# Performance work log

Measured on AMD Instinct MI355X. Metric: run time of the kernel, lower is better.

## Reference

```python
import jax, jax.numpy as jnp
import numpy as np

N_NODES = 50000
N_EDGES = 800000
D_IN = 64
D_HID = 64
N_LAYERS = 3
BN_EPS = 1e-5


def setup_inputs() -> dict:
    key = jax.random.key(0)
    ks = jax.random.split(key, 10)
    x = jax.random.normal(ks[0], (N_NODES, D_IN), dtype=jnp.float32)
    edge_index = jax.random.randint(ks[1], (2, N_EDGES), 0, N_NODES, dtype=jnp.int32)
    # Per-layer GCN weights (in==hid==64 so we can stack) and BatchNorm params.
    Ws = jax.random.normal(ks[2], (N_LAYERS, D_HID, D_HID), dtype=jnp.float32) / np.sqrt(D_HID)
    bs = jnp.zeros((N_LAYERS, D_HID), dtype=jnp.float32)
    gammas = jnp.ones((N_LAYERS, D_HID), dtype=jnp.float32)
    betas = jnp.zeros((N_LAYERS, D_HID), dtype=jnp.float32)
    means = jax.random.normal(ks[3], (N_LAYERS, D_HID), dtype=jnp.float32) * 0.1
    variances = jax.random.uniform(ks[4], (N_LAYERS, D_HID), dtype=jnp.float32, minval=0.5, maxval=1.5)
    lin_w = jax.random.normal(ks[5], (D_HID, 1), dtype=jnp.float32) / np.sqrt(D_HID)
    lin_b = jnp.zeros((1,), dtype=jnp.float32)
    return {"x": x, "edge_index": edge_index, "Ws": Ws, "bs": bs,
            "gammas": gammas, "betas": betas, "means": means,
            "variances": variances, "lin_w": lin_w, "lin_b": lin_b}


def _gnn_forward(x, edge_index, Ws, bs, gammas, betas, means, variances, lin_w, lin_b):
    n = x.shape[0]
    # GCNConv: add self loops, symmetric D^{-1/2}(A+I)D^{-1/2} normalization.
    loop = jnp.arange(n, dtype=edge_index.dtype)
    row = jnp.concatenate([edge_index[0], loop])  # source nodes
    col = jnp.concatenate([edge_index[1], loop])  # target nodes
    deg = jax.ops.segment_sum(jnp.ones(row.shape[0], x.dtype), col, num_segments=n)
    dinv = jax.lax.rsqrt(jnp.maximum(deg, 1.0))  # deg >= 1 from self loops
    norm = (dinv[row] * dinv[col])[:, None]  # [E+N, 1]

    h = x
    for i in range(N_LAYERS):
        h = h @ Ws[i]  # transform first (PyG GCNConv order)
        h = jax.ops.segment_sum(h[row] * norm, col, num_segments=n) + bs[i]
        # BatchNorm1d (eval mode: running stats) + ReLU; dropout is identity in eval.
        h = (h - means[i]) * jax.lax.rsqrt(variances[i] + BN_EPS) * gammas[i] + betas[i]
        h = jax.nn.relu(h)
    out = h @ lin_w + lin_b  # [N, 1]
    return out[:, 0]


def reference(x, edge_index, Ws, bs, gammas, betas, means, variances, lin_w, lin_b):
    return _gnn_forward(x, edge_index, Ws, bs, gammas, betas, means, variances, lin_w, lin_b)
```

## Files before the change

kernel.cpp:

```cpp
#include <hip/hip_runtime.h>
#include <hip/hip_bf16.h>
#include <hip/hip_fp16.h>


#define BN_EPS 1e-5f
#define CAP 64
#define CHUNK 4096
#define SEGCAP 5120
#define NBINS_MAX 256

__global__ __launch_bounds__(256) void k_bin_pairs(const int* __restrict__ row,
                                                   const int* __restrict__ col,
                                                   int* __restrict__ gfill,
                                                   unsigned int* __restrict__ gpairs,
                                                   int e, int nbins) {
    __shared__ unsigned int pl[CHUNK];
    __shared__ int bcnt[NBINS_MAX];
    __shared__ int bbase[NBINS_MAX];
    int tid = threadIdx.x;
    int base = blockIdx.x * CHUNK;
    for (int b = tid; b < nbins; b += 256) bcnt[b] = 0;
    __syncthreads();
    int nloc = e - base; if (nloc > CHUNK) nloc = CHUNK;
    #pragma unroll
    for (int it = 0; it < CHUNK / 1024; ++it) {
        int le = (it * 256 + tid) * 4;
        if (le + 3 < nloc) {
            int i4 = (base >> 2) + it * 256 + tid;
            int4 r = ((const int4*)row)[i4];
            int4 c = ((const int4*)col)[i4];
            atomicAdd(&bcnt[c.x >> 8], 1); pl[le + 0] = (unsigned)r.x | ((unsigned)c.x << 16);
            atomicAdd(&bcnt[c.y >> 8], 1); pl[le + 1] = (unsigned)r.y | ((unsigned)c.y << 16);
            atomicAdd(&bcnt[c.z >> 8], 1); pl[le + 2] = (unsigned)r.z | ((unsigned)c.z << 16);
            atomicAdd(&bcnt[c.w >> 8], 1); pl[le + 3] = (unsigned)r.w | ((unsigned)c.w << 16);
        } else {
            for (int j = 0; j < 4; ++j) {
                if (le + j < nloc) {
                    int rr = row[base + le + j];
                    int cc = col[base + le + j];
                    atomicAdd(&bcnt[cc >> 8], 1);
                    pl[le + j] = (unsigned)rr | ((unsigned)cc << 16);
                }
            }
        }
    }
    __syncthreads();
    for (int b = tid; b < nbins; b += 256) {
        bbase[b] = atomicAdd(&gfill[b], bcnt[b]);
        bcnt[b] = 0;
    }
    __syncthreads();
    for (int i = tid; i < nloc; i += 256) {
        unsigned int p = pl[i];
        int bin = p >> 24;
        int off = atomicAdd(&bcnt[bin], 1);
        int pos = bbase[bin] + off;
        if (pos < SEGCAP) gpairs[(size_t)bin * SEGCAP + pos] = p;
    }
}

__global__ __launch_bounds__(256) void k_bucket_build(const unsigned int* __restrict__ gpairs,
                                                      const int* __restrict__ gfill,
                                                      int* __restrict__ cnt,
                                                      unsigned short* __restrict__ bucket,
                                                      int n) {
    __shared__ unsigned short lb[256 * CAP];
    __shared__ int lc[256];
    int tid = threadIdx.x;
    int bin = blockIdx.x;
    lc[tid] = 0;
    __syncthreads();
    int m = gfill[bin]; if (m > SEGCAP) m = SEGCAP;
    const unsigned int* seg = gpairs + (size_t)bin * SEGCAP;
    for (int i = tid; i < m; i += 256) {
        unsigned int p = seg[i];
        int src = p & 0xffff;
        int dl = (p >> 16) & 255;
        int pos = atomicAdd(&lc[dl], 1);
        if (pos < CAP) lb[dl * CAP + pos] = (unsigned short)src;
    }
    __syncthreads();
    int nodebase = bin << 8;
    const int4* lb4 = (const int4*)lb;
    int4* gb4 = (int4*)bucket;
    for (int i = tid; i < 256 * 8; i += 256) {
        int rrow = i >> 3;
        int gnode = nodebase + rrow;
        if (gnode < n) gb4[(size_t)gnode * 8 + (i & 7)] = lb4[i];
    }
    int gnode = nodebase + tid;
    if (gnode < n) cnt[gnode] = lc[tid];
}

__device__ __forceinline__ void mm_core(const float* at, const float* wsh,
                                        __half* out, int rbase, int n, int tid) {
    int r = tid >> 2;
    int cg = tid & 3;
    float4 a0 = {0, 0, 0, 0}, a1 = a0, a2 = a0, a3 = a0;
    const float4* W4 = (const float4*)wsh;
    #pragma unroll 8
    for (int k = 0; k < 64; ++k) {
        float hv = at[k * 65 + r];
        float4 w0 = W4[k * 16 + cg * 4 + 0];
        float4 w1 = W4[k * 16 + cg * 4 + 1];
        float4 w2 = W4[k * 16 + cg * 4 + 2];
        float4 w3 = W4[k * 16 + cg * 4 + 3];
        a0.x = fmaf(hv, w0.x, a0.x); a0.y = fmaf(hv, w0.y, a0.y);
        a0.z = fmaf(hv, w0.z, a0.z); a0.w = fmaf(hv, w0.w, a0.w);
        a1.x = fmaf(hv, w1.x, a1.x); a1.y = fmaf(hv, w1.y, a1.y);
        a1.z = fmaf(hv, w1.z, a1.z); a1.w = fmaf(hv, w1.w, a1.w);
        a2.x = fmaf(hv, w2.x, a2.x); a2.y = fmaf(hv, w2.y, a2.y);
        a2.z = fmaf(hv, w2.z, a2.z); a2.w = fmaf(hv, w2.w, a2.w);
        a3.x = fmaf(hv, w3.x, a3.x); a3.y = fmaf(hv, w3.y, a3.y);
        a3.z = fmaf(hv, w3.z, a3.z); a3.w = fmaf(hv, w3.w, a3.w);
    }
    int gr = rbase + r;
    if (gr < n) {
        union { __half2 h2[4]; uint4 u; } o1, o2;
        o1.h2[0] = __floats2half2_rn(a0.x, a0.y);
        o1.h2[1] = __floats2half2_rn(a0.z, a0.w);
        o1.h2[2] = __floats2half2_rn(a1.x, a1.y);
        o1.h2[3] = __floats2half2_rn(a1.z, a1.w);
        o2.h2[0] = __floats2half2_rn(a2.x, a2.y);
        o2.h2[1] = __floats2half2_rn(a2.z, a2.w);
        o2.h2[2] = __floats2half2_rn(a3.x, a3.y);
        o2.h2[3] = __floats2half2_rn(a3.z, a3.w);
        uint4* op = (uint4*)(out + (size_t)gr * 64 + cg * 16);
        op[0] = o1.u; op[1] = o2.u;
    }
}

template<int LAYER>
__global__ __launch_bounds__(256) void k_mm(const __half* __restrict__ A,
                                            const float* __restrict__ W,
                                            __half* __restrict__ out, int n) {
    __shared__ float at[64 * 65];
    __shared__ float wsh[64 * 64];
    int tid = threadIdx.x;
    int rbase = blockIdx.x * 64;
    for (int i = tid; i < 4096; i += 256) wsh[i] = W[i];
    for (int i = tid; i < 2048; i += 256) {
        int r = i >> 5;
        int c2 = (i & 31) * 2;
        int gr = rbase + r;
        float2 v = {0.f, 0.f};
        if (gr < n) v = __half22float2(*(const __half2*)(A + (size_t)gr * 64 + c2));
        at[c2 * 65 + r] = v.x;
        at[(c2 + 1) * 65 + r] = v.y;
    }
    __syncthreads();
    mm_core(at, wsh, out, rbase, n, tid);
}

__global__ __launch_bounds__(256) void k_mm0(const float* __restrict__ A,
                                             const float* __restrict__ W,
                                             const int* __restrict__ cnt,
                                             __half* __restrict__ out, int n) {
    __shared__ float at[64 * 65];
    __shared__ float wsh[64 * 64];
    __shared__ float dl[64];
    int tid = threadIdx.x;
    int rbase = blockIdx.x * 64;
    if (tid < 64) {
        int gr = rbase + tid;
        dl[tid] = (gr < n) ? rsqrtf((float)(cnt[gr] + 1)) : 0.f;
    }
    for (int i = tid; i < 4096; i += 256) wsh[i] = W[i];
    __syncthreads();
    for (int i = tid; i < 1024; i += 256) {
        int r = i >> 4;
        int c4 = (i & 15) * 4;
        int gr = rbase + r;
        float4 v = {0.f, 0.f, 0.f, 0.f};
        if (gr < n) v = *(const float4*)(A + (size_t)gr * 64 + c4);
        float d = dl[r];
        at[(c4 + 0) * 65 + r] = v.x * d;
        at[(c4 + 1) * 65 + r] = v.y * d;
        at[(c4 + 2) * 65 + r] = v.z * d;
        at[(c4 + 3) * 65 + r] = v.w * d;
    }
    __syncthreads();
    mm_core(at, wsh, out, rbase, n, tid);
}

template<int LAYER, bool FINAL>
__global__ __launch_bounds__(256, 6) void k_agg(const __half* __restrict__ t,
                                                const int* __restrict__ cnt,
                                                const unsigned short* __restrict__ bucket,
                                                const float* __restrict__ bias,
                                                const float* __restrict__ gamma,
                                                const float* __restrict__ beta,
                                                const float* __restrict__ mean,
                                                const float* __restrict__ var,
                                                __half* __restrict__ hout,
                                                const float* __restrict__ lw,
                                                const float* __restrict__ lb,
                                                float* __restrict__ outp, int n) {
    int lane = threadIdx.x & 63;
    int g = lane >> 3;
    int q = lane & 7;
    int qo = q << 3;
    float S[8], O[8], LW[8];
    #pragma unroll
    for (int i = 0; i < 8; ++i) {
        int f = qo + i;
        float s = gamma[f] * rsqrtf(var[f] + BN_EPS);
        S[i] = s;
        O[i] = fmaf(bias[f] - mean[f], s, beta[f]);
        if (FINAL) LW[i] = lw[f];
    }
    int wave = (blockIdx.x * blockDim.x + threadIdx.x) >> 6;
    int nwaves = (gridDim.x * blockDim.x) >> 6;
    union HV { float4 f4; __half2 h2[4]; };
    for (int node = wave; node < n; node += nwaves) {
        int c = cnt[node];
        int myidx = (int)bucket[node * CAP + lane];
        HV vself;
        vself.f4 = *(const float4*)(t + ((size_t)node << 6) + qo);
        float acc[8] = {0.f, 0.f, 0.f, 0.f, 0.f, 0.f, 0.f, 0.f};
        int cm1 = c - 1;
        for (int sub = 0; sub < c; sub += 16) {
            int j1 = sub + g;
            int j2 = sub + 8 + g;
            int i1 = __shfl(myidx, (j1 < cm1 ? j1 : cm1), 64);
            int i2 = __shfl(myidx, (j2 < cm1 ? j2 : cm1), 64);
            float m1 = (j1 < c) ? 1.f : 0.f;
            float m2 = (j2 < c) ? 1.f : 0.f;
            HV v1, v2;
            v1.f4 = *(const float4*)(t + ((size_t)i1 << 6) + qo);
            v2.f4 = *(const float4*)(t + ((size_t)i2 << 6) + qo);
            #pragma unroll
            for (int p = 0; p < 4; ++p) {
                float2 a = __half22float2(v1.h2[p]);
                float2 b = __half22float2(v2.h2[p]);
                acc[2 * p]     = fmaf(m1, a.x, acc[2 * p]);
                acc[2 * p + 1] = fmaf(m1, a.y, acc[2 * p + 1]);
                acc[2 * p]     = fmaf(m2, b.x, acc[2 * p]);
                acc[2 * p + 1] = fmaf(m2, b.y, acc[2 * p + 1]);
            }
        }
        {
            float ms = (g == 0) ? 1.f : 0.f;
            #pragma unroll
            for (int p = 0; p < 4; ++p) {
                float2 a = __half22float2(vself.h2[p]);
                acc[2 * p]     = fmaf(ms, a.x, acc[2 * p]);
                acc[2 * p + 1] = fmaf(ms, a.y, acc[2 * p + 1]);
            }
        }
        #pragma unroll
        for (int i = 0; i < 8; ++i) {
            acc[i] += __shfl_down(acc[i], 32, 64);
            acc[i] += __shfl_down(acc[i], 16, 64);
            acc[i] += __shfl_down(acc[i], 8, 64);
        }
        float di = rsqrtf((float)(c + 1));
        if (FINAL) {
            float p = 0.f;
            #pragma unroll
            for (int i = 0; i < 8; ++i) {
                float h = fmaxf(fmaf(acc[i] * di, S[i], O[i]), 0.f);
                p = fmaf(h, LW[i], p);
            }
            p += __shfl_down(p, 4, 64);
            p += __shfl_down(p, 2, 64);
            p += __shfl_down(p, 1, 64);
            if (lane == 0) outp[node] = p + lb[0];
        } else if (g == 0) {
            union { __half2 h2[4]; uint4 u; } o;
            #pragma unroll
            for (int i = 0; i < 4; ++i) {
                float h0 = fmaxf(fmaf(acc[2 * i] * di, S[2 * i], O[2 * i]), 0.f);
                float h1 = fmaxf(fmaf(acc[2 * i + 1] * di, S[2 * i + 1], O[2 * i + 1]), 0.f);
                o.h2[i] = __floats2half2_rn(h0 * di, h1 * di);
            }
            *(uint4*)(hout + ((size_t)node << 6) + qo) = o.u;
        }
    }
}

extern "C" void kernel_launch(void* const* d_in, const int* in_sizes, int n_in,
                              void* d_out, int out_size, void* d_ws, size_t ws_size,
                              hipStream_t stream) {
    const float* x    = (const float*)d_in[0];
    const int*   ei   = (const int*)d_in[1];
    const float* Ws   = (const float*)d_in[2];
    const float* bs   = (const float*)d_in[3];
    const float* gam  = (const float*)d_in[4];
    const float* bet  = (const float*)d_in[5];
    const float* mean = (const float*)d_in[6];
    const float* var  = (const float*)d_in[7];
    const float* lw   = (const float*)d_in[8];
    const float* lb   = (const float*)d_in[9];
    float* out = (float*)d_out;

    const int n = in_sizes[0] / 64;
    const int e = in_sizes[1] / 2;
    const int* row = ei;
    const int* col = ei + e;
    const int nbins = (n + 255) >> 8;

    int* ws_i = (int*)d_ws;
    int* cnt = ws_i;
    int* gfill = ws_i + n;
    unsigned short* bucket = (unsigned short*)(ws_i + n + 256);
    __half* t16 = (__half*)(ws_i + n + 256 + 32 * (size_t)n);
    __half* h16 = t16 + 64 * (size_t)n;
    unsigned int* gpairs = (unsigned int*)t16;

    int nb_p1 = (e + CHUNK - 1) / CHUNK;
    int nb_mm = (n + 63) / 64;
    int nb_ag = 2048;

    hipMemsetAsync(gfill, 0, 256 * sizeof(int), stream);
    k_bin_pairs<<<nb_p1, 256, 0, stream>>>(row, col, gfill, gpairs, e, nbins);
    k_bucket_build<<<nbins, 256, 0, stream>>>(gpairs, gfill, cnt, bucket, n);

    k_mm0<<<nb_mm, 256, 0, stream>>>(x, Ws, cnt, t16, n);
    k_agg<0, false><<<nb_ag, 256, 0, stream>>>(t16, cnt, bucket,
                                               bs, gam, bet, mean, var,
                                               h16, nullptr, nullptr, nullptr, n);
    k_mm<1><<<nb_mm, 256, 0, stream>>>(h16, Ws + 4096, t16, n);
    k_agg<1, false><<<nb_ag, 256, 0, stream>>>(t16, cnt, bucket,
                                               bs + 64, gam + 64, bet + 64, mean + 64, var + 64,
                                               h16, nullptr, nullptr, nullptr, n);
    k_mm<2><<<nb_mm, 256, 0, stream>>>(h16, Ws + 8192, t16, n);
    k_agg<2, true><<<nb_ag, 256, 0, stream>>>(t16, cnt, bucket,
                                              bs + 128, gam + 128, bet + 128, mean + 128, var + 128,
                                              nullptr, lw, lb, out, n);
}
```

Before: 230.3 us.

## Replace scalar FMA node-transform GEMMs with split-fp16 MFMA kernels

Replaces the shared-memory scalar-FMA 64x64 transform kernels with a matrix-core kernel using 16x16x32 fp16 MFMA instructions. A small prep kernel converts each layer's weights to transposed hi/lo fp16 pairs, and the first layer also splits the fp32 input into hi/lo to keep near-fp32 accuracy. This removes the LDS staging and transpose and cuts the per-row FMA work. The cost is extra MFMAs for the split precision, scalar fp16 output stores, and per-lane weight fragments read from global memory.

```diff
diff --git a/kernel.cpp b/kernel.cpp
--- a/kernel.cpp
+++ b/kernel.cpp
@@ -8,6 +8,9 @@
 #define CHUNK 4096
 #define SEGCAP 5120
 #define NBINS_MAX 256
+
+typedef _Float16 f16x8 __attribute__((ext_vector_type(8)));
+typedef float f32x4 __attribute__((ext_vector_type(4)));
 
 __global__ __launch_bounds__(256) void k_bin_pairs(const int* __restrict__ row,
                                                    const int* __restrict__ col,
@@ -92,95 +95,97 @@
     if (gnode < n) cnt[gnode] = lc[tid];
 }
 
-__device__ __forceinline__ void mm_core(const float* at, const float* wsh,
-                                        __half* out, int rbase, int n, int tid) {
-    int r = tid >> 2;
-    int cg = tid & 3;
-    float4 a0 = {0, 0, 0, 0}, a1 = a0, a2 = a0, a3 = a0;
-    const float4* W4 = (const float4*)wsh;
-    #pragma unroll 8
-    for (int k = 0; k < 64; ++k) {
-        float hv = at[k * 65 + r];
-        float4 w0 = W4[k * 16 + cg * 4 + 0];
-        float4 w1 = W4[k * 16 + cg * 4 + 1];
-        float4 w2 = W4[k * 16 + cg * 4 + 2];
-        float4 w3 = W4[k * 16 + cg * 4 + 3];
-        a0.x = fmaf(hv, w0.x, a0.x); a0.y = fmaf(hv, w0.y, a0.y);
-        a0.z = fmaf(hv, w0.z, a0.z); a0.w = fmaf(hv, w0.w, a0.w);
-        a1.x = fmaf(hv, w1.x, a1.x); a1.y = fmaf(hv, w1.y, a1.y);
-        a1.z = fmaf(hv, w1.z, a1.z); a1.w = fmaf(hv, w1.w, a1.w);
-        a2.x = fmaf(hv, w2.x, a2.x); a2.y = fmaf(hv, w2.y, a2.y);
-        a2.z = fmaf(hv, w2.z, a2.z); a2.w = fmaf(hv, w2.w, a2.w);
-        a3.x = fmaf(hv, w3.x, a3.x); a3.y = fmaf(hv, w3.y, a3.y);
-        a3.z = fmaf(hv, w3.z, a3.z); a3.w = fmaf(hv, w3.w, a3.w);
-    }
-    int gr = rbase + r;
-    if (gr < n) {
-        union { __half2 h2[4]; uint4 u; } o1, o2;
-        o1.h2[0] = __floats2half2_rn(a0.x, a0.y);
-        o1.h2[1] = __floats2half2_rn(a0.z, a0.w);
-        o1.h2[2] = __floats2half2_rn(a1.x, a1.y);
-        o1.h2[3] = __floats2half2_rn(a1.z, a1.w);
-        o2.h2[0] = __floats2half2_rn(a2.x, a2.y);
-        o2.h2[1] = __floats2half2_rn(a2.z, a2.w);
-        o2.h2[2] = __floats2half2_rn(a3.x, a3.y);
-        o2.h2[3] = __floats2half2_rn(a3.z, a3.w);
-        uint4* op = (uint4*)(out + (size_t)gr * 64 + cg * 16);
-        op[0] = o1.u; op[1] = o2.u;
-    }
-}
-
-template<int LAYER>
-__global__ __launch_bounds__(256) void k_mm(const __half* __restrict__ A,
-                                            const float* __restrict__ W,
-                                            __half* __restrict__ out, int n) {
-    __shared__ float at[64 * 65];
-    __shared__ float wsh[64 * 64];
+__global__ __launch_bounds__(256) void k_wprep(const float* __restrict__ Ws,
+                                               __half* __restrict__ wt) {
+    int l = blockIdx.x;
     int tid = threadIdx.x;
-    int rbase = blockIdx.x * 64;
-    for (int i = tid; i < 4096; i += 256) wsh[i] = W[i];
-    for (int i = tid; i < 2048; i += 256) {
-        int r = i >> 5;
-        int c2 = (i & 31) * 2;
-        int gr = rbase + r;
-        float2 v = {0.f, 0.f};
-        if (gr < n) v = __half22float2(*(const __half2*)(A + (size_t)gr * 64 + c2));
-        at[c2 * 65 + r] = v.x;
-        at[(c2 + 1) * 65 + r] = v.y;
-    }
-    __syncthreads();
-    mm_core(at, wsh, out, rbase, n, tid);
-}
-
-__global__ __launch_bounds__(256) void k_mm0(const float* __restrict__ A,
-                                             const float* __restrict__ W,
-                                             const int* __restrict__ cnt,
-                                             __half* __restrict__ out, int n) {
-    __shared__ float at[64 * 65];
-    __shared__ float wsh[64 * 64];
-    __shared__ float dl[64];
+    const float* W = Ws + l * 4096;
+    __half* hi = wt + (size_t)l * 8192;
+    __half* lo = hi + 4096;
+    for (int i = tid; i < 4096; i += 256) {
+        int k = i >> 6, nn = i & 63;
+        float w = W[k * 64 + nn];
+        __half h = __float2half_rn(w);
+        hi[nn * 64 + k] = h;
+        lo[nn * 64 + k] = __float2half_rn(w - __half2float(h));
+    }
+}
+
+template<bool L0>
+__global__ __launch_bounds__(256) void k_mm_mfma(const void* __restrict__ Ain,
+                                                 const __half* __restrict__ wt,
+                                                 const int* __restrict__ cnt,
+                                                 __half* __restrict__ out, int n) {
     int tid = threadIdx.x;
-    int rbase = blockIdx.x * 64;
-    if (tid < 64) {
-        int gr = rbase + tid;
-        dl[tid] = (gr < n) ? rsqrtf((float)(cnt[gr] + 1)) : 0.f;
-    }
-    for (int i = tid; i < 4096; i += 256) wsh[i] = W[i];
-    __syncthreads();
-    for (int i = tid; i < 1024; i += 256) {
-        int r = i >> 4;
-        int c4 = (i & 15) * 4;
-        int gr = rbase + r;
-        float4 v = {0.f, 0.f, 0.f, 0.f};
-        if (gr < n) v = *(const float4*)(A + (size_t)gr * 64 + c4);
-        float d = dl[r];
-        at[(c4 + 0) * 65 + r] = v.x * d;
-        at[(c4 + 1) * 65 + r] = v.y * d;
-        at[(c4 + 2) * 65 + r] = v.z * d;
-        at[(c4 + 3) * 65 + r] = v.w * d;
-    }
-    __syncthreads();
-    mm_core(at, wsh, out, rbase, n, tid);
+    int w = tid >> 6;
+    int lane = tid & 63;
+    int r = lane & 15;
+    int kg = lane >> 4;
+    int row = blockIdx.x * 64 + w * 16 + r;
+    bool inb = row < n;
+
+    f16x8 ahi0 = {}, ahi1 = {}, alo0 = {}, alo1 = {};
+    if (L0) {
+        const float* A = (const float*)Ain;
+        if (inb) {
+            float di = rsqrtf((float)(cnt[row] + 1));
+            const float4* ap0 = (const float4*)(A + (size_t)row * 64 + kg * 8);
+            const float4* ap1 = (const float4*)(A + (size_t)row * 64 + 32 + kg * 8);
+            float4 v0 = ap0[0], v1 = ap0[1];
+            float4 v2 = ap1[0], v3 = ap1[1];
+            float f[16] = {v0.x, v0.y, v0.z, v0.w, v1.x, v1.y, v1.z, v1.w,
+                           v2.x, v2.y, v2.z, v2.w, v3.x, v3.y, v3.z, v3.w};
+            #pragma unroll
+            for (int i = 0; i < 8; ++i) {
+                float s0 = f[i] * di, s1 = f[8 + i] * di;
+                _Float16 h0 = (_Float16)s0, h1 = (_Float16)s1;
+                ahi0[i] = h0; ahi1[i] = h1;
+                alo0[i] = (_Float16)(s0 - (float)h0);
+                alo1[i] = (_Float16)(s1 - (float)h1);
+            }
+        }
+    } else {
+        const __half* A = (const __half*)Ain;
+        if (inb) {
+            union { uint4 u; f16x8 h; } u0, u1;
+            u0.u = *(const uint4*)(A + (size_t)row * 64 + kg * 8);
+            u1.u = *(const uint4*)(A + (size_t)row * 64 + 32 + kg * 8);
+            ahi0 = u0.h; ahi1 = u1.h;
+        }
+    }
+
+    const __half* whi = wt;
+    const __half* wlo = wt + 4096;
+    f32x4 acc[4];
+    #pragma unroll
+    for (int t = 0; t < 4; ++t) {
+        int cb = t * 16 + r;
+        union { uint4 u; f16x8 h; } bh0, bh1, bl0, bl1;
+        bh0.u = *(const uint4*)(whi + cb * 64 + kg * 8);
+        bh1.u = *(const uint4*)(whi + cb * 64 + 32 + kg * 8);
+        bl0.u = *(const uint4*)(wlo + cb * 64 + kg * 8);
+        bl1.u = *(const uint4*)(wlo + cb * 64 + 32 + kg * 8);
+        f32x4 a = {0.f, 0.f, 0.f, 0.f};
+        a = __builtin_amdgcn_mfma_f32_16x16x32_f16(ahi0, bh0.h, a, 0, 0, 0);
+        a = __builtin_amdgcn_mfma_f32_16x16x32_f16(ahi1, bh1.h, a, 0, 0, 0);
+        a = __builtin_amdgcn_mfma_f32_16x16x32_f16(ahi0, bl0.h, a, 0, 0, 0);
+        a = __builtin_amdgcn_mfma_f32_16x16x32_f16(ahi1, bl1.h, a, 0, 0, 0);
+        if (L0) {
+            a = __builtin_amdgcn_mfma_f32_16x16x32_f16(alo0, bh0.h, a, 0, 0, 0);
+            a = __builtin_amdgcn_mfma_f32_16x16x32_f16(alo1, bh1.h, a, 0, 0, 0);
+        }
+        acc[t] = a;
+    }
+
+    int orow_base = blockIdx.x * 64 + w * 16 + 4 * kg;
+    #pragma unroll
+    for (int t = 0; t < 4; ++t) {
+        #pragma unroll
+        for (int i = 0; i < 4; ++i) {
+            int orow = orow_base + i;
+            if (orow < n) out[(size_t)orow * 64 + t * 16 + r] = __float2half_rn(acc[t][i]);
+        }
+    }
 }
 
 template<int LAYER, bool FINAL>
@@ -306,6 +311,7 @@
     unsigned short* bucket = (unsigned short*)(ws_i + n + 256);
     __half* t16 = (__half*)(ws_i + n + 256 + 32 * (size_t)n);
     __half* h16 = t16 + 64 * (size_t)n;
+    __half* wt = (__half*)(((uintptr_t)(h16 + 64 * (size_t)n) + 15) & ~(uintptr_t)15);
     unsigned int* gpairs = (unsigned int*)t16;
 
     int nb_p1 = (e + CHUNK - 1) / CHUNK;
@@ -313,18 +319,19 @@
     int nb_ag = 2048;
 
     hipMemsetAsync(gfill, 0, 256 * sizeof(int), stream);
+    k_wprep<<<3, 256, 0, stream>>>(Ws, wt);
     k_bin_pairs<<<nb_p1, 256, 0, stream>>>(row, col, gfill, gpairs, e, nbins);
     k_bucket_build<<<nbins, 256, 0, stream>>>(gpairs, gfill, cnt, bucket, n);
 
-    k_mm0<<<nb_mm, 256, 0, stream>>>(x, Ws, cnt, t16, n);
+    k_mm_mfma<true><<<nb_mm, 256, 0, stream>>>(x, wt, cnt, t16, n);
     k_agg<0, false><<<nb_ag, 256, 0, stream>>>(t16, cnt, bucket,
                                                bs, gam, bet, mean, var,
                                                h16, nullptr, nullptr, nullptr, n);
-    k_mm<1><<<nb_mm, 256, 0, stream>>>(h16, Ws + 4096, t16, n);
+    k_mm_mfma<false><<<nb_mm, 256, 0, stream>>>(h16, wt + 8192, cnt, t16, n);
     k_agg<1, false><<<nb_ag, 256, 0, stream>>>(t16, cnt, bucket,
                                                bs + 64, gam + 64, bet + 64, mean + 64, var + 64,
                                                h16, nullptr, nullptr, nullptr, n);
-    k_mm<2><<<nb_mm, 256, 0, stream>>>(h16, Ws + 8192, t16, n);
+    k_mm_mfma<false><<<nb_mm, 256, 0, stream>>>(h16, wt + 16384, cnt, t16, n);
     k_agg<2, true><<<nb_ag, 256, 0, stream>>>(t16, cnt, bucket,
                                               bs + 128, gam + 128, bet + 128, mean + 128, var + 128,
                                               nullptr, lw, lb, out, n);
```

Result: faster. 225.2 us (-2.2%).
